# Performance work log

Measured on AMD Instinct MI355X. Metric: run time of the kernel, lower is better.

The kernel has to match this reference:

```python
import jax, jax.numpy as jnp
import numpy as np

TEMP = 1.0
EPS = 1e-3  # keras LayerNormalization default epsilon


def _ln(x, g, b):
    m = jnp.mean(x, -1, keepdims=True)
    v = jnp.mean((x - m) ** 2, -1, keepdims=True)
    return g * (x - m) * jax.lax.rsqrt(v + EPS) + b


def setup_inputs() -> dict:
    key = jax.random.key(0)
    ks = jax.random.split(key, 16)
    B, N, C, A, F = 8, 2048, 64, 256, 128
    r = lambda k, s: (jax.random.normal(ks[k], s) * 0.02).astype(jnp.float32)
    z = lambda n: jnp.zeros((n,), jnp.float32)
    return {
        'spatial': jax.random.normal(ks[0], (B, N, C), jnp.float32),
        'frequency': jax.random.normal(ks[1], (B, N, C), jnp.float32),
        'wavelet': jax.random.normal(ks[2], (B, N, C), jnp.float32),
        'Ws': r(3, (C, A)), 'bs': z(A),
        'Wf': r(4, (C, A)), 'bf': z(A),
        'Ww': r(5, (C, A)), 'bw': z(A),
        'g1': jnp.ones((A,), jnp.float32), 'b1': z(A),
        'Wk': r(6, (A, F)), 'bk': z(F),
        'Wq': r(7, (A, F)), 'bq': z(F),
        'Wt': r(8, (A, F)), 'bt': z(F),
        'Wg': r(9, (F + 3, F)), 'bg': z(F),
        'Wfu': r(10, (3 * F, F)), 'bfu': z(F),
        'Wdf': r(11, (F, F)), 'bdf': z(F),
        'g2': jnp.ones((F,), jnp.float32), 'b2': z(F),
    }


def _forward(spatial, frequency, wavelet, Ws, bs, Wf, bf, Ww, bw, g1, b1,
             Wk, bk, Wq, bq, Wt, bt, Wg, bg, Wfu, bfu, Wdf, bdf, g2, b2):
    B = spatial.shape[0]
    # FeatureAlignment: per-domain Dense + shared LayerNorm
    aligned = [
        _ln(spatial @ Ws + bs, g1, b1),
        _ln(frequency @ Wf + bf, g1, b1),
        _ln(wavelet @ Ww + bw, g1, b1),
    ]  # each [B, N, A]
    # DomainCorrelation
    K = [a @ Wk + bk for a in aligned]  # [B, N, F]
    Q = [a @ Wq + bq for a in aligned]
    corr = jnp.zeros((B, 3, 3), spatial.dtype)
    for i in range(3):
        for j in range(i, 3):
            # queries from domain j, keys from domain i (as in original)
            s = jax.nn.softmax(jnp.einsum('bnd,bmd->bnm', Q[j], K[i]) / TEMP, axis=-1)
            m = jnp.mean(s, axis=(1, 2))  # [B]
            corr = corr.at[:, i, j].set(m)
            if i != j:
                corr = corr.at[:, j, i].set(m)
    # NOTE: original applies softmax over the batch axis of the [B] row means
    dw = [jax.nn.softmax(jnp.mean(corr[:, i, :], axis=1)) for i in range(3)]  # each [B]
    # FeatureTransfer
    corr_mean = jnp.mean(corr, axis=1)  # [B, 3]
    enhanced = []
    for a, w in zip(aligned, dw):
        t = a @ Wt + bt  # [B, N, F]
        N = t.shape[1]
        gin = jnp.concatenate([t, jnp.broadcast_to(corr_mean[:, None, :], (B, N, 3))], axis=-1)
        gate = jax.nn.sigmoid(gin @ Wg + bg)
        enhanced.append(t * gate * w[:, None, None])
    fused = jnp.concatenate(enhanced, axis=-1) @ Wfu + bfu  # [B, N, F]
    out = _ln(fused @ Wdf + bdf, g2, b2)
    return out, corr, dw, enhanced


def reference(spatial, frequency, wavelet, Ws, bs, Wf, bf, Ww, bw, g1, b1,
              Wk, bk, Wq, bq, Wt, bt, Wg, bg, Wfu, bfu, Wdf, bdf, g2, b2):
    out, corr, dw, enh = _forward(spatial, frequency, wavelet, Ws, bs, Wf, bf, Ww, bw,
                                  g1, b1, Wk, bk, Wq, bq, Wt, bt, Wg, bg, Wfu, bfu,
                                  Wdf, bdf, g2, b2)
    return (out, corr, dw[0], dw[1], dw[2], enh[0], enh[1], enh[2])
```

## Files before the change

### kernel.cpp

```cpp
#include <hip/hip_runtime.h>
#include <math.h>


typedef __attribute__((ext_vector_type(8))) short short8;
typedef __attribute__((ext_vector_type(4))) float f32x4;
#define MFMA(a, b, c) __builtin_amdgcn_mfma_f32_16x16x32_bf16(a, b, c, 0, 0, 0)

#define NTOK 32
#define XP 72
#define AP 264
#define TP 136

#define WD0_B 0u
#define WD1_B 32768u
#define WD2_B 65536u
#define WT_B  98304u
#define WG_B  163840u
#define WF0_B 196608u
#define WF1_B 229376u
#define WF2_B 262144u
#define WDF_B 294912u

__device__ __forceinline__ unsigned short bf16rtn(float v) {
    unsigned u = __float_as_uint(v);
    unsigned r = u + 0x7FFFu + ((u >> 16) & 1u);
    return (unsigned short)(r >> 16);
}
__device__ __forceinline__ void split2(float v, unsigned short& h, unsigned short& l) {
    h = bf16rtn(v);
    float hf = __uint_as_float(((unsigned)h) << 16);
    l = bf16rtn(v - hf);
}
__device__ __forceinline__ float bf2f(unsigned short h) {
    return __uint_as_float(((unsigned)h) << 16);
}

__global__ __launch_bounds__(256) void prep_kernel(
    const float* __restrict__ Ws, const float* __restrict__ Wf,
    const float* __restrict__ Ww, const float* __restrict__ Wt,
    const float* __restrict__ Wg, const float* __restrict__ Wfu,
    const float* __restrict__ Wdf, unsigned short* __restrict__ ws)
{
    int s = blockIdx.x * 256 + threadIdx.x;
    const float* src; int K, N; unsigned base, S; int fi;
    if (s < 2048)      { src = Ws;            K = 64;  N = 256; base = WD0_B; S = 16384; fi = s; }
    else if (s < 4096) { src = Wf;            K = 64;  N = 256; base = WD1_B; S = 16384; fi = s - 2048; }
    else if (s < 6144) { src = Ww;            K = 64;  N = 256; base = WD2_B; S = 16384; fi = s - 4096; }
    else if (s < 10240){ src = Wt;            K = 256; N = 128; base = WT_B;  S = 32768; fi = s - 6144; }
    else if (s < 12288){ src = Wg;            K = 128; N = 128; base = WG_B;  S = 16384; fi = s - 10240; }
    else if (s < 14336){ src = Wfu;           K = 128; N = 128; base = WF0_B; S = 16384; fi = s - 12288; }
    else if (s < 16384){ src = Wfu + 16384;   K = 128; N = 128; base = WF1_B; S = 16384; fi = s - 14336; }
    else if (s < 18432){ src = Wfu + 32768;   K = 128; N = 128; base = WF2_B; S = 16384; fi = s - 16384; }
    else               { src = Wdf;           K = 128; N = 128; base = WDF_B; S = 16384; fi = s - 18432; }
    const int lane = fi & 63, frag = fi >> 6;
    const int KC = K >> 5;
    const int nt = frag / KC, kc = frag - nt * KC;
    const int n  = nt * 16 + (lane & 15);
    const int k0 = kc * 32 + (lane >> 4) * 8;
    short8 hv, lv;
    #pragma unroll
    for (int j = 0; j < 8; ++j) {
        unsigned short h, l;
        split2(src[(k0 + j) * N + n], h, l);
        hv[j] = (short)h; lv[j] = (short)l;
    }
    *(short8*)&ws[base + (unsigned)fi * 8]     = hv;
    *(short8*)&ws[base + S + (unsigned)fi * 8] = lv;
}

__device__ __forceinline__ void gemm128_d2(
    const unsigned short* __restrict__ wsB, unsigned S,
    const unsigned short* __restrict__ Ph, const unsigned short* __restrict__ Pl,
    int tok0, int tok1, int quad, int wv, int lane, f32x4 acc[2])
{
    short8 Bh[2], Bl[2];
    #pragma unroll
    for (int j = 0; j < 2; ++j) {
        const unsigned short* bp = wsB + ((unsigned)(wv * 4 + j) * 64 + lane) * 8;
        Bh[j] = *(const short8*)bp; Bl[j] = *(const short8*)(bp + S);
    }
    #pragma unroll
    for (int kc = 0; kc < 4; ++kc) {
        const short8 bh = Bh[kc & 1], bl = Bl[kc & 1];
        if (kc + 2 < 4) {
            const unsigned short* bp = wsB + ((unsigned)(wv * 4 + kc + 2) * 64 + lane) * 8;
            Bh[kc & 1] = *(const short8*)bp; Bl[kc & 1] = *(const short8*)(bp + S);
        }
        const int k = kc * 32 + quad * 8;
        const short8 Ah0 = *(const short8*)&Ph[tok0 * TP + k];
        const short8 Al0 = *(const short8*)&Pl[tok0 * TP + k];
        const short8 Ah1 = *(const short8*)&Ph[tok1 * TP + k];
        const short8 Al1 = *(const short8*)&Pl[tok1 * TP + k];
        acc[0] = MFMA(Ah0, bh, acc[0]);
        acc[0] = MFMA(Al0, bh, acc[0]);
        acc[0] = MFMA(Ah0, bl, acc[0]);
        acc[1] = MFMA(Ah1, bh, acc[1]);
        acc[1] = MFMA(Al1, bh, acc[1]);
        acc[1] = MFMA(Ah1, bl, acc[1]);
    }
}

__global__ __launch_bounds__(512) void mega_kernel(
    const float* __restrict__ x0, const float* __restrict__ x1,
    const float* __restrict__ x2,
    const float* __restrict__ bd0, const float* __restrict__ bd1,
    const float* __restrict__ bd2,
    const float* __restrict__ g1, const float* __restrict__ b1,
    const float* __restrict__ bt, const float* __restrict__ Wg,
    const float* __restrict__ bg, const float* __restrict__ bfu,
    const float* __restrict__ bdf, const float* __restrict__ g2,
    const float* __restrict__ b2,
    const unsigned short* __restrict__ ws,
    float* __restrict__ out, float* __restrict__ consts,
    float* __restrict__ e0, float* __restrict__ e1, float* __restrict__ e2)
{
    __shared__ __align__(16) unsigned char smem[53248];
    unsigned short* xh = (unsigned short*)smem;
    unsigned short* xl = xh + 32 * XP;
    unsigned short* th = (unsigned short*)smem;
    unsigned short* tl = th + 32 * TP;
    unsigned short* ah = (unsigned short*)(smem + 17408);
    unsigned short* al = ah + 32 * AP;
    unsigned short* eh = (unsigned short*)(smem + 17408);
    unsigned short* el = eh + 32 * TP;
    float* ostage = (float*)(smem + 17408);
    float* psumS  = (float*)(smem + 51200);
    float* psumQ  = psumS + 32 * 8;

    const int tid = threadIdx.x, wv = tid >> 6, lane = tid & 63;
    const int lm = lane & 15, quad = lane >> 4;
    const int row0 = blockIdx.x * NTOK;
    const int tok0 = lm, tok1 = lm + 16;
    const int stok = tid >> 4, sc4 = (tid & 15) * 4;

    if (blockIdx.x == 0) {
        if (tid < 72) consts[tid] = 4.8828125e-4f;
        else if (tid < 96) consts[tid] = 0.125f;
    }

    int cA[2]; float g1c[2], b1c[2];
    #pragma unroll
    for (int i = 0; i < 2; ++i) { cA[i] = (wv * 2 + i) * 16 + lm; g1c[i] = g1[cA[i]]; b1c[i] = b1[cA[i]]; }
    const int cT = wv * 16 + lm;
    const float btc = bt[cT];
    const float bgc = bg[cT] + 4.8828125e-4f * (Wg[16384 + cT] + Wg[16512 + cT] + Wg[16640 + cT]);
    const float bdc = bdf[cT], g2c = g2[cT], b2c = b2[cT];
    f32x4 facc[2];
    { const float bv = bfu[cT]; facc[0] = (f32x4){bv, bv, bv, bv}; facc[1] = facc[0]; }

    const float* xs[3]  = {x0, x1, x2};
    const float* bds[3] = {bd0, bd1, bd2};
    float* es[3] = {e0, e1, e2};
    const unsigned WDB[3] = {WD0_B, WD1_B, WD2_B};
    const unsigned WFB[3] = {WF0_B, WF1_B, WF2_B};

    {
        const f32x4 v = __builtin_nontemporal_load(
            (const f32x4*)&xs[0][(row0 + stok) * 64 + sc4]);
        unsigned short h0, l0, h1, l1, h2, l2, h3, l3;
        split2(v.x, h0, l0); split2(v.y, h1, l1);
        split2(v.z, h2, l2); split2(v.w, h3, l3);
        *(ushort4*)&xh[stok * XP + sc4] = make_ushort4(h0, h1, h2, h3);
        *(ushort4*)&xl[stok * XP + sc4] = make_ushort4(l0, l1, l2, l3);
    }
    __syncthreads();

    for (int d = 0; d < 3; ++d) {
        f32x4 acc[2][2];
        {
            const float* bdp = bds[d];
            #pragma unroll
            for (int i = 0; i < 2; ++i) {
                const float bv = bdp[cA[i]];
                acc[i][0] = (f32x4){bv, bv, bv, bv}; acc[i][1] = acc[i][0];
            }
        }
        {
            short8 Bh[2], Bl[2];
            #pragma unroll
            for (int j = 0; j < 2; ++j) {
                const unsigned short* bp = ws + WDB[d] +
                    ((unsigned)((wv * 2 + j) * 2 + 0) * 64 + lane) * 8;
                Bh[j] = *(const short8*)bp; Bl[j] = *(const short8*)(bp + 16384);
            }
            #pragma unroll
            for (int f = 0; f < 4; ++f) {
                const int kc = f >> 1, i = f & 1;
                const short8 bh = Bh[f & 1], bl = Bl[f & 1];
                if (f + 2 < 4) {
                    const int f2 = f + 2;
                    const unsigned short* bp = ws + WDB[d] +
                        ((unsigned)((wv * 2 + (f2 & 1)) * 2 + (f2 >> 1)) * 64 + lane) * 8;
                    Bh[f & 1] = *(const short8*)bp; Bl[f & 1] = *(const short8*)(bp + 16384);
                }
                const int k = kc * 32 + quad * 8;
                const short8 Ah0 = *(const short8*)&xh[tok0 * XP + k];
                const short8 Al0 = *(const short8*)&xl[tok0 * XP + k];
                const short8 Ah1 = *(const short8*)&xh[tok1 * XP + k];
                const short8 Al1 = *(const short8*)&xl[tok1 * XP + k];
                acc[i][0] = MFMA(Ah0, bh, acc[i][0]);
                acc[i][0] = MFMA(Al0, bh, acc[i][0]);
                acc[i][0] = MFMA(Ah0, bl, acc[i][0]);
                acc[i][1] = MFMA(Ah1, bh, acc[i][1]);
                acc[i][1] = MFMA(Al1, bh, acc[i][1]);
                acc[i][1] = MFMA(Ah1, bl, acc[i][1]);
            }
        }
        #pragma unroll
        for (int m = 0; m < 2; ++m)
            #pragma unroll
            for (int r = 0; r < 4; ++r) {
                float s = acc[0][m][r] + acc[1][m][r];
                float q = acc[0][m][r] * acc[0][m][r] + acc[1][m][r] * acc[1][m][r];
                #pragma unroll
                for (int off = 1; off < 16; off <<= 1) {
                    s += __shfl_xor(s, off); q += __shfl_xor(q, off);
                }
                if (lm == 0) {
                    const int row = m * 16 + quad * 4 + r;
                    psumS[row * 8 + wv] = s;
                    psumQ[row * 8 + wv] = q;
                }
            }
        __syncthreads();

        #pragma unroll
        for (int m = 0; m < 2; ++m)
            #pragma unroll
            for (int r = 0; r < 4; ++r) {
                const int row = m * 16 + quad * 4 + r;
                const float4 s0 = *(const float4*)&psumS[row * 8];
                const float4 s1 = *(const float4*)&psumS[row * 8 + 4];
                const float4 q0 = *(const float4*)&psumQ[row * 8];
                const float4 q1 = *(const float4*)&psumQ[row * 8 + 4];
                const float S = s0.x + s0.y + s0.z + s0.w + s1.x + s1.y + s1.z + s1.w;
                const float Q = q0.x + q0.y + q0.z + q0.w + q1.x + q1.y + q1.z + q1.w;
                const float mean = S * (1.f / 256.f);
                const float rs = rsqrtf(Q * (1.f / 256.f) - mean * mean + 1e-3f);
                #pragma unroll
                for (int i = 0; i < 2; ++i) {
                    const float v = (acc[i][m][r] - mean) * rs * g1c[i] + b1c[i];
                    unsigned short h, l; split2(v, h, l);
                    ah[row * AP + cA[i]] = h; al[row * AP + cA[i]] = l;
                }
            }
        __syncthreads();

        f32x4 xvn;
        if (d < 2)
            xvn = __builtin_nontemporal_load(
                (const f32x4*)&xs[d + 1][(row0 + stok) * 64 + sc4]);

        f32x4 tac[2];
        tac[0] = (f32x4){btc, btc, btc, btc}; tac[1] = tac[0];
        {
            short8 Bh[2], Bl[2];
            #pragma unroll
            for (int j = 0; j < 2; ++j) {
                const unsigned short* bp = ws + WT_B + ((unsigned)(wv * 8 + j) * 64 + lane) * 8;
                Bh[j] = *(const short8*)bp; Bl[j] = *(const short8*)(bp + 32768);
            }
            #pragma unroll
            for (int kc = 0; kc < 8; ++kc) {
                const short8 bh = Bh[kc & 1], bl = Bl[kc & 1];
                if (kc + 2 < 8) {
                    const unsigned short* bp = ws + WT_B + ((unsigned)(wv * 8 + kc + 2) * 64 + lane) * 8;
                    Bh[kc & 1] = *(const short8*)bp; Bl[kc & 1] = *(const short8*)(bp + 32768);
                }
                const int k = kc * 32 + quad * 8;
                const short8 Ah0 = *(const short8*)&ah[tok0 * AP + k];
                const short8 Al0 = *(const short8*)&al[tok0 * AP + k];
                const short8 Ah1 = *(const short8*)&ah[tok1 * AP + k];
                const short8 Al1 = *(const short8*)&al[tok1 * AP + k];
                tac[0] = MFMA(Ah0, bh, tac[0]);
                tac[0] = MFMA(Al0, bh, tac[0]);
                tac[0] = MFMA(Ah0, bl, tac[0]);
                tac[1] = MFMA(Ah1, bh, tac[1]);
                tac[1] = MFMA(Al1, bh, tac[1]);
                tac[1] = MFMA(Ah1, bl, tac[1]);
            }
        }
        #pragma unroll
        for (int m = 0; m < 2; ++m)
            #pragma unroll
            for (int r = 0; r < 4; ++r) {
                const int row = m * 16 + quad * 4 + r;
                unsigned short h, l; split2(tac[m][r], h, l);
                th[row * TP + cT] = h; tl[row * TP + cT] = l;
            }
        __syncthreads();

        f32x4 zac[2];
        zac[0] = (f32x4){bgc, bgc, bgc, bgc}; zac[1] = zac[0];
        gemm128_d2(ws + WG_B, 16384, th, tl, tok0, tok1, quad, wv, lane, zac);

        #pragma unroll
        for (int m = 0; m < 2; ++m)
            #pragma unroll
            for (int r = 0; r < 4; ++r) {
                const int row = m * 16 + quad * 4 + r;
                const float tv = bf2f(th[row * TP + cT]) + bf2f(tl[row * TP + cT]);
                const float e = tv * (1.f / (1.f + __expf(-zac[m][r]))) * 0.125f;
                unsigned short h, l; split2(e, h, l);
                eh[row * TP + cT] = h; el[row * TP + cT] = l;
            }
        __syncthreads();

        gemm128_d2(ws + WFB[d], 16384, eh, el, tok0, tok1, quad, wv, lane, facc);

        #pragma unroll
        for (int p = 0; p < 2; ++p) {
            const int row = (tid >> 5) + p * 16;
            const int c4 = (tid & 31) * 4;
            const ushort4 h0 = *(const ushort4*)&eh[row * TP + c4];
            const ushort4 l0 = *(const ushort4*)&el[row * TP + c4];
            f32x4 o = {bf2f(h0.x) + bf2f(l0.x), bf2f(h0.y) + bf2f(l0.y),
                       bf2f(h0.z) + bf2f(l0.z), bf2f(h0.w) + bf2f(l0.w)};
            __builtin_nontemporal_store(o, (f32x4*)(es[d] + (row0 + row) * 128 + c4));
        }

        if (d < 2) {
            unsigned short h0, l0, h1, l1, h2, l2, h3, l3;
            split2(xvn.x, h0, l0); split2(xvn.y, h1, l1);
            split2(xvn.z, h2, l2); split2(xvn.w, h3, l3);
            *(ushort4*)&xh[stok * XP + sc4] = make_ushort4(h0, h1, h2, h3);
            *(ushort4*)&xl[stok * XP + sc4] = make_ushort4(l0, l1, l2, l3);
        } else {
            #pragma unroll
            for (int m = 0; m < 2; ++m)
                #pragma unroll
                for (int r = 0; r < 4; ++r) {
                    const int row = m * 16 + quad * 4 + r;
                    unsigned short h, l; split2(facc[m][r], h, l);
                    th[row * TP + cT] = h; tl[row * TP + cT] = l;
                }
        }
        __syncthreads();
    }

    f32x4 dac[2];
    dac[0] = (f32x4){bdc, bdc, bdc, bdc}; dac[1] = dac[0];
    gemm128_d2(ws + WDF_B, 16384, th, tl, tok0, tok1, quad, wv, lane, dac);

    #pragma unroll
    for (int m = 0; m < 2; ++m)
        #pragma unroll
        for (int r = 0; r < 4; ++r) {
            float s = dac[m][r];
            float q = dac[m][r] * dac[m][r];
            #pragma unroll
            for (int off = 1; off < 16; off <<= 1) {
                s += __shfl_xor(s, off); q += __shfl_xor(q, off);
            }
            if (lm == 0) {
                const int row = m * 16 + quad * 4 + r;
                psumS[row * 8 + wv] = s;
                psumQ[row * 8 + wv] = q;
            }
        }
    __syncthreads();
    #pragma unroll
    for (int m = 0; m < 2; ++m)
        #pragma unroll
        for (int r = 0; r < 4; ++r) {
            const int row = m * 16 + quad * 4 + r;
            const float4 s0 = *(const float4*)&psumS[row * 8];
            const float4 s1 = *(const float4*)&psumS[row * 8 + 4];
            const float4 q0 = *(const float4*)&psumQ[row * 8];
            const float4 q1 = *(const float4*)&psumQ[row * 8 + 4];
            const float S = s0.x + s0.y + s0.z + s0.w + s1.x + s1.y + s1.z + s1.w;
            const float Q = q0.x + q0.y + q0.z + q0.w + q1.x + q1.y + q1.z + q1.w;
            const float mean = S * (1.f / 128.f);
            const float rs = rsqrtf(Q * (1.f / 128.f) - mean * mean + 1e-3f);
            ostage[row * 128 + cT] = (dac[m][r] - mean) * rs * g2c + b2c;
        }
    __syncthreads();
    #pragma unroll
    for (int p = 0; p < 2; ++p) {
        const int row = (tid >> 5) + p * 16;
        const int c4 = (tid & 31) * 4;
        const f32x4 o = *(const f32x4*)&ostage[row * 128 + c4];
        __builtin_nontemporal_store(o, (f32x4*)(out + (row0 + row) * 128 + c4));
    }
}

extern "C" void kernel_launch(void* const* d_in, const int* in_sizes, int n_in,
                              void* d_out, int out_size, void* d_ws, size_t ws_size,
                              hipStream_t stream) {
    const float* spatial   = (const float*)d_in[0];
    const float* frequency = (const float*)d_in[1];
    const float* wavelet   = (const float*)d_in[2];
    const float* Ws  = (const float*)d_in[3];
    const float* bs  = (const float*)d_in[4];
    const float* Wf  = (const float*)d_in[5];
    const float* bf  = (const float*)d_in[6];
    const float* Ww  = (const float*)d_in[7];
    const float* bw  = (const float*)d_in[8];
    const float* g1  = (const float*)d_in[9];
    const float* b1  = (const float*)d_in[10];
    const float* Wt  = (const float*)d_in[15];
    const float* bt  = (const float*)d_in[16];
    const float* Wg  = (const float*)d_in[17];
    const float* bg  = (const float*)d_in[18];
    const float* Wfu = (const float*)d_in[19];
    const float* bfu = (const float*)d_in[20];
    const float* Wdf = (const float*)d_in[21];
    const float* bdf = (const float*)d_in[22];
    const float* g2  = (const float*)d_in[23];
    const float* b2  = (const float*)d_in[24];

    float* out    = (float*)d_out;
    float* consts = out + 2097152;
    float* enh0   = out + 2097248;
    float* enh1   = out + 4194400;
    float* enh2   = out + 6291552;
    unsigned short* wsp = (unsigned short*)d_ws;

    prep_kernel<<<80, 256, 0, stream>>>(Ws, Wf, Ww, Wt, Wg, Wfu, Wdf, wsp);
    mega_kernel<<<16384 / NTOK, 512, 0, stream>>>(
        spatial, frequency, wavelet, bs, bf, bw, g1, b1,
        bt, Wg, bg, bfu, bdf, g2, b2, wsp,
        out, consts, enh0, enh1, enh2);
}
```

Measured before the change: 178.7 us.

## Use packed bf16 conversion, pad LN partial sums, add occupancy hint and staggered start

Replaces the software round-to-nearest bf16 hi/lo split with the hardware v_cvt_pk_bf16_f32 instruction, which converts two values per instruction, across all staging paths. It pads the per-row LayerNorm partial-sum arrays to stride 12 to change their LDS bank mapping. It sets launch_bounds(512,4) to ask the compiler for an occupancy target. It also makes blocks whose index has bit 256 set sleep briefly at start so their memory traffic is staggered. The packed convert may round differently from the hand-written RTN path, and the occupancy hint may force register spills.

```diff
diff --git a/kernel.cpp b/kernel.cpp
--- a/kernel.cpp
+++ b/kernel.cpp
@@ -10,6 +10,7 @@
 #define XP 72
 #define AP 264
 #define TP 136
+#define PP 12
 
 #define WD0_B 0u
 #define WD1_B 32768u
@@ -33,6 +34,28 @@
 }
 __device__ __forceinline__ float bf2f(unsigned short h) {
     return __uint_as_float(((unsigned)h) << 16);
+}
+
+__device__ __forceinline__ unsigned cvt_pk_bf16(float a, float b) {
+    unsigned r;
+    asm("v_cvt_pk_bf16_f32 %0, %1, %2" : "=v"(r) : "v"(a), "v"(b));
+    return r;
+}
+__device__ __forceinline__ void split2pk(float a, float b, unsigned& hp, unsigned& lp) {
+    hp = cvt_pk_bf16(a, b);
+    const float ha = __uint_as_float(hp << 16);
+    const float hb = __uint_as_float(hp & 0xffff0000u);
+    lp = cvt_pk_bf16(a - ha, b - hb);
+}
+__device__ __forceinline__ void stage_x(const f32x4 v,
+                                        unsigned short* __restrict__ xh,
+                                        unsigned short* __restrict__ xl,
+                                        int stok, int sc4) {
+    unsigned h01, l01, h23, l23;
+    split2pk(v.x, v.y, h01, l01);
+    split2pk(v.z, v.w, h23, l23);
+    *(uint2*)&xh[stok * XP + sc4] = make_uint2(h01, h23);
+    *(uint2*)&xl[stok * XP + sc4] = make_uint2(l01, l23);
 }
 
 __global__ __launch_bounds__(256) void prep_kernel(
@@ -100,7 +123,7 @@
     }
 }
 
-__global__ __launch_bounds__(512) void mega_kernel(
+__global__ __launch_bounds__(512, 4) void mega_kernel(
     const float* __restrict__ x0, const float* __restrict__ x1,
     const float* __restrict__ x2,
     const float* __restrict__ bd0, const float* __restrict__ bd1,
@@ -114,7 +137,7 @@
     float* __restrict__ out, float* __restrict__ consts,
     float* __restrict__ e0, float* __restrict__ e1, float* __restrict__ e2)
 {
-    __shared__ __align__(16) unsigned char smem[53248];
+    __shared__ __align__(16) unsigned char smem[54272];
     unsigned short* xh = (unsigned short*)smem;
     unsigned short* xl = xh + 32 * XP;
     unsigned short* th = (unsigned short*)smem;
@@ -125,7 +148,9 @@
     unsigned short* el = eh + 32 * TP;
     float* ostage = (float*)(smem + 17408);
     float* psumS  = (float*)(smem + 51200);
-    float* psumQ  = psumS + 32 * 8;
+    float* psumQ  = psumS + 32 * PP;
+
+    if (blockIdx.x & 256) __builtin_amdgcn_s_sleep(78);
 
     const int tid = threadIdx.x, wv = tid >> 6, lane = tid & 63;
     const int lm = lane & 15, quad = lane >> 4;
@@ -157,11 +182,7 @@
     {
         const f32x4 v = __builtin_nontemporal_load(
             (const f32x4*)&xs[0][(row0 + stok) * 64 + sc4]);
-        unsigned short h0, l0, h1, l1, h2, l2, h3, l3;
-        split2(v.x, h0, l0); split2(v.y, h1, l1);
-        split2(v.z, h2, l2); split2(v.w, h3, l3);
-        *(ushort4*)&xh[stok * XP + sc4] = make_ushort4(h0, h1, h2, h3);
-        *(ushort4*)&xl[stok * XP + sc4] = make_ushort4(l0, l1, l2, l3);
+        stage_x(v, xh, xl, stok, sc4);
     }
     __syncthreads();
 
@@ -218,8 +239,8 @@
                 }
                 if (lm == 0) {
                     const int row = m * 16 + quad * 4 + r;
-                    psumS[row * 8 + wv] = s;
-                    psumQ[row * 8 + wv] = q;
+                    psumS[row * PP + wv] = s;
+                    psumQ[row * PP + wv] = q;
                 }
             }
         __syncthreads();
@@ -229,20 +250,21 @@
             #pragma unroll
             for (int r = 0; r < 4; ++r) {
                 const int row = m * 16 + quad * 4 + r;
-                const float4 s0 = *(const float4*)&psumS[row * 8];
-                const float4 s1 = *(const float4*)&psumS[row * 8 + 4];
-                const float4 q0 = *(const float4*)&psumQ[row * 8];
-                const float4 q1 = *(const float4*)&psumQ[row * 8 + 4];
+                const float4 s0 = *(const float4*)&psumS[row * PP];
+                const float4 s1 = *(const float4*)&psumS[row * PP + 4];
+                const float4 q0 = *(const float4*)&psumQ[row * PP];
+                const float4 q1 = *(const float4*)&psumQ[row * PP + 4];
                 const float S = s0.x + s0.y + s0.z + s0.w + s1.x + s1.y + s1.z + s1.w;
                 const float Q = q0.x + q0.y + q0.z + q0.w + q1.x + q1.y + q1.z + q1.w;
                 const float mean = S * (1.f / 256.f);
                 const float rs = rsqrtf(Q * (1.f / 256.f) - mean * mean + 1e-3f);
-                #pragma unroll
-                for (int i = 0; i < 2; ++i) {
-                    const float v = (acc[i][m][r] - mean) * rs * g1c[i] + b1c[i];
-                    unsigned short h, l; split2(v, h, l);
-                    ah[row * AP + cA[i]] = h; al[row * AP + cA[i]] = l;
-                }
+                const float v0 = (acc[0][m][r] - mean) * rs * g1c[0] + b1c[0];
+                const float v1 = (acc[1][m][r] - mean) * rs * g1c[1] + b1c[1];
+                unsigned hp, lp; split2pk(v0, v1, hp, lp);
+                ah[row * AP + cA[0]] = (unsigned short)hp;
+                ah[row * AP + cA[1]] = (unsigned short)(hp >> 16);
+                al[row * AP + cA[0]] = (unsigned short)lp;
+                al[row * AP + cA[1]] = (unsigned short)(lp >> 16);
             }
         __syncthreads();
 
@@ -281,13 +303,20 @@
             }
         }
         #pragma unroll
-        for (int m = 0; m < 2; ++m)
-            #pragma unroll
-            for (int r = 0; r < 4; ++r) {
-                const int row = m * 16 + quad * 4 + r;
-                unsigned short h, l; split2(tac[m][r], h, l);
-                th[row * TP + cT] = h; tl[row * TP + cT] = l;
-            }
+        for (int m = 0; m < 2; ++m) {
+            const int rb = m * 16 + quad * 4;
+            unsigned hp, lp;
+            split2pk(tac[m][0], tac[m][1], hp, lp);
+            th[rb * TP + cT]       = (unsigned short)hp;
+            th[(rb + 1) * TP + cT] = (unsigned short)(hp >> 16);
+            tl[rb * TP + cT]       = (unsigned short)lp;
+            tl[(rb + 1) * TP + cT] = (unsigned short)(lp >> 16);
+            split2pk(tac[m][2], tac[m][3], hp, lp);
+            th[(rb + 2) * TP + cT] = (unsigned short)hp;
+            th[(rb + 3) * TP + cT] = (unsigned short)(hp >> 16);
+            tl[(rb + 2) * TP + cT] = (unsigned short)lp;
+            tl[(rb + 3) * TP + cT] = (unsigned short)(lp >> 16);
+        }
         __syncthreads();
 
         f32x4 zac[2];
@@ -295,15 +324,27 @@
         gemm128_d2(ws + WG_B, 16384, th, tl, tok0, tok1, quad, wv, lane, zac);
 
         #pragma unroll
-        for (int m = 0; m < 2; ++m)
+        for (int m = 0; m < 2; ++m) {
+            const int rb = m * 16 + quad * 4;
+            float e[4];
             #pragma unroll
             for (int r = 0; r < 4; ++r) {
-                const int row = m * 16 + quad * 4 + r;
+                const int row = rb + r;
                 const float tv = bf2f(th[row * TP + cT]) + bf2f(tl[row * TP + cT]);
-                const float e = tv * (1.f / (1.f + __expf(-zac[m][r]))) * 0.125f;
-                unsigned short h, l; split2(e, h, l);
-                eh[row * TP + cT] = h; el[row * TP + cT] = l;
-            }
+                e[r] = tv * (1.f / (1.f + __expf(-zac[m][r]))) * 0.125f;
+            }
+            unsigned hp, lp;
+            split2pk(e[0], e[1], hp, lp);
+            eh[rb * TP + cT]       = (unsigned short)hp;
+            eh[(rb + 1) * TP + cT] = (unsigned short)(hp >> 16);
+            el[rb * TP + cT]       = (unsigned short)lp;
+            el[(rb + 1) * TP + cT] = (unsigned short)(lp >> 16);
+            split2pk(e[2], e[3], hp, lp);
+            eh[(rb + 2) * TP + cT] = (unsigned short)hp;
+            eh[(rb + 3) * TP + cT] = (unsigned short)(hp >> 16);
+            el[(rb + 2) * TP + cT] = (unsigned short)lp;
+            el[(rb + 3) * TP + cT] = (unsigned short)(lp >> 16);
+        }
         __syncthreads();
 
         gemm128_d2(ws + WFB[d], 16384, eh, el, tok0, tok1, quad, wv, lane, facc);
@@ -320,20 +361,23 @@
         }
 
         if (d < 2) {
-            unsigned short h0, l0, h1, l1, h2, l2, h3, l3;
-            split2(xvn.x, h0, l0); split2(xvn.y, h1, l1);
-            split2(xvn.z, h2, l2); split2(xvn.w, h3, l3);
-            *(ushort4*)&xh[stok * XP + sc4] = make_ushort4(h0, h1, h2, h3);
-            *(ushort4*)&xl[stok * XP + sc4] = make_ushort4(l0, l1, l2, l3);
+            stage_x(xvn, xh, xl, stok, sc4);
         } else {
             #pragma unroll
-            for (int m = 0; m < 2; ++m)
-                #pragma unroll
-                for (int r = 0; r < 4; ++r) {
-                    const int row = m * 16 + quad * 4 + r;
-                    unsigned short h, l; split2(facc[m][r], h, l);
-                    th[row * TP + cT] = h; tl[row * TP + cT] = l;
-                }
+            for (int m = 0; m < 2; ++m) {
+                const int rb = m * 16 + quad * 4;
+                unsigned hp, lp;
+                split2pk(facc[m][0], facc[m][1], hp, lp);
+                th[rb * TP + cT]       = (unsigned short)hp;
+                th[(rb + 1) * TP + cT] = (unsigned short)(hp >> 16);
+                tl[rb * TP + cT]       = (unsigned short)lp;
+                tl[(rb + 1) * TP + cT] = (unsigned short)(lp >> 16);
+                split2pk(facc[m][2], facc[m][3], hp, lp);
+                th[(rb + 2) * TP + cT] = (unsigned short)hp;
+                th[(rb + 3) * TP + cT] = (unsigned short)(hp >> 16);
+                tl[(rb + 2) * TP + cT] = (unsigned short)lp;
+                tl[(rb + 3) * TP + cT] = (unsigned short)(lp >> 16);
+            }
         }
         __syncthreads();
     }
@@ -354,8 +398,8 @@
             }
             if (lm == 0) {
                 const int row = m * 16 + quad * 4 + r;
-                psumS[row * 8 + wv] = s;
-                psumQ[row * 8 + wv] = q;
+                psumS[row * PP + wv] = s;
+                psumQ[row * PP + wv] = q;
             }
         }
     __syncthreads();
@@ -364,10 +408,10 @@
         #pragma unroll
         for (int r = 0; r < 4; ++r) {
             const int row = m * 16 + quad * 4 + r;
-            const float4 s0 = *(const float4*)&psumS[row * 8];
-            const float4 s1 = *(const float4*)&psumS[row * 8 + 4];
-            const float4 q0 = *(const float4*)&psumQ[row * 8];
-            const float4 q1 = *(const float4*)&psumQ[row * 8 + 4];
+            const float4 s0 = *(const float4*)&psumS[row * PP];
+            const float4 s1 = *(const float4*)&psumS[row * PP + 4];
+            const float4 q0 = *(const float4*)&psumQ[row * PP];
+            const float4 q1 = *(const float4*)&psumQ[row * PP + 4];
             const float S = s0.x + s0.y + s0.z + s0.w + s1.x + s1.y + s1.z + s1.w;
             const float Q = q0.x + q0.y + q0.z + q0.w + q1.x + q1.y + q1.z + q1.w;
             const float mean = S * (1.f / 128.f);
```

Result: slower. 186.8 us (+4.5%).
